# Performance work log

Measured on AMD Instinct MI355X. Metric: run time of the kernel, lower is better.

Reference implementation:

```python
import jax, jax.numpy as jnp
import numpy as np

EPS = 1e-8

def setup_inputs() -> dict:
    key = jax.random.key(0)
    k1, k2, k3 = jax.random.split(key, 3)
    b, c, h, w = 64, 20, 128, 128
    x = jax.random.normal(k1, (b, c, h, w), dtype=jnp.float32)
    y = jax.random.randint(k2, (b, c), 0, 2).astype(jnp.int32)
    threshold_p = jnp.zeros((b, c, h * w), dtype=jnp.float32)
    fg = jax.random.uniform(k3, (b, c), dtype=jnp.float32)
    return {"x": x, "y": y, "threshold_p": threshold_p, "fg": fg, "iter": 0}

def reference(x, y, threshold_p, fg, iter):
    b, c, h, w = x.shape
    hw = h * w
    xs = jax.nn.sigmoid(x.reshape(b, c, hw))  # [b,c,hw]
    yf = y.astype(xs.dtype)
    if iter % 100 < 80:
        # per-row descending sort, pick the fg*(h*w)-th value as threshold
        srt = -jnp.sort(-xs.reshape(b * c, hw), axis=1)  # descending
        idx = (fg.reshape(-1) * hw).astype(jnp.int32)  # [b*c]
        thr = jnp.take_along_axis(srt, idx[:, None], axis=1).reshape(b, c, 1)
        thr = jax.lax.stop_gradient(thr)
    else:
        thr = jax.nn.sigmoid(jnp.mean(threshold_p.reshape(b, c, hw), axis=2))[:, :, None]
        xs = jax.lax.stop_gradient(xs)
    thr = jnp.clip(thr, 0.0001)  # [b,c,1], broadcasts over hw
    y_ = yf[:, :, None]  # [b,c,1] broadcast equivalent of stacking hw copies
    mask_low = jax.lax.stop_gradient((xs <= thr).astype(xs.dtype) * y_)
    mask_high = jax.lax.stop_gradient((xs > thr).astype(xs.dtype) * y_)
    h_low = (-(xs * xs) / (thr * thr) + 2.0 * xs / thr) * mask_low
    alpha = 1.0 / jnp.clip((1.0 - thr) ** 2, EPS)
    h_high = alpha * (1.0 - xs) * (1.0 - 2.0 * thr + xs) * mask_high
    if iter % 100 < 80:
        neg_loss = -(1.0 - y_) * jnp.log(jnp.clip(1.0 - xs, EPS))
        loss = jnp.mean(h_high + h_low + neg_loss)
    else:
        loss = jnp.sum(h_low) / jnp.sum(mask_low) + jnp.sum(h_high) / jnp.sum(mask_high)
    return loss
```

## Files before the change

kernel.cpp:

```cpp
#include <hip/hip_runtime.h>

#define HW     16384
#define NROWS  1280
#define CAPH   1024
#define MB     256

__device__ __forceinline__ unsigned f2u(float f) {
    unsigned u = __float_as_uint(f);
    unsigned m = (unsigned)((int)u >> 31);
    return u ^ (m | 0x80000000u);
}
__device__ __forceinline__ float u2f(unsigned u) {
    u = (u & 0x80000000u) ? (u & 0x7fffffffu) : ~u;
    return __uint_as_float(u);
}

__device__ __forceinline__ float norminv(float p) {
    const float a1=-3.969683028665376e+01f,a2=2.209460984245205e+02f,
                a3=-2.759285104469687e+02f,a4=1.383577518672690e+02f,
                a5=-3.066479806614716e+01f,a6=2.506628277459239e+00f;
    const float b1=-5.447609879822406e+01f,b2=1.615858368580409e+02f,
                b3=-1.556989798598866e+02f,b4=6.680131188771972e+01f,
                b5=-1.328068155288572e+01f;
    const float c1=-7.784894002430293e-03f,c2=-3.223964580411365e-01f,
                c3=-2.400758277161838e+00f,c4=-2.549732539343734e+00f,
                c5=4.374664141464968e+00f,c6=2.938163982698783e+00f;
    const float d1=7.784695709041462e-03f,d2=3.224671290700398e-01f,
                d3=2.445134137142996e+00f,d4=3.754408661907416e+00f;
    const float plow = 0.02425f;
    float q, r;
    if (p < plow) {
        q = sqrtf(-2.f * logf(p));
        return (((((c1*q+c2)*q+c3)*q+c4)*q+c5)*q+c6) /
               ((((d1*q+d2)*q+d3)*q+d4)*q+1.f);
    } else if (p <= 1.f - plow) {
        q = p - 0.5f; r = q * q;
        return (((((a1*r+a2)*r+a3)*r+a4)*r+a5)*r+a6)*q /
               (((((b1*r+b2)*r+b3)*r+b4)*r+b5)*r+1.f);
    } else {
        q = sqrtf(-2.f * logf(1.f - p));
        return -(((((c1*q+c2)*q+c3)*q+c4)*q+c5)*q+c6) /
                ((((d1*q+d2)*q+d3)*q+d4)*q+1.f);
    }
}

__device__ __forceinline__ void bracket_ab(int k, float* fa, float* fb) {
    const float pq  = 1.f - ((float)k + 0.5f) * (1.f / (float)HW);
    const float z   = norminv(pq);
    const float phi = 0.39894228f * exp2f(-0.72134752f * z * z);
    const float sig = sqrtf(pq * (1.f - pq) * (1.f / (float)HW)) / phi;
    const float dl  = 6.f * sig + 0.02f;
    *fa = z + dl; *fb = z - dl;
}

template<int NTH>
__device__ __forceinline__ void block_scan_pick(
    const unsigned* h, int bpl, int stride, unsigned kk,
    volatile unsigned* s_bin, volatile unsigned* s_k, unsigned* wtot)
{
    constexpr int NW = NTH / 64;
    const int tid  = threadIdx.x;
    const int lane = tid & 63;
    const int wid  = tid >> 6;
    const int base = tid * bpl;
    unsigned local = 0;
    for (int j = 0; j < bpl; ++j) {
        int b = base + j;
        local += h[stride * b] + (stride == 2 ? h[stride * b + 1] : 0u);
    }
    unsigned s = local;
    #pragma unroll
    for (int off = 1; off < 64; off <<= 1) {
        unsigned t = __shfl_down(s, off, 64);
        if (lane + off < 64) s += t;
    }
    if (lane == 0) wtot[wid] = s;
    __syncthreads();
    unsigned aw = 0;
    #pragma unroll
    for (int w = 0; w < NW; ++w) if (w > wid) aw += wtot[w];
    const unsigned above = aw + (s - local);
    if (above <= kk && above + local > kk) {
        unsigned run = above;
        for (int j = bpl - 1; j >= 0; --j) {
            int b = base + j;
            unsigned c = h[stride * b] + (stride == 2 ? h[stride * b + 1] : 0u);
            if (run + c > kk) { *s_bin = (unsigned)b; *s_k = kk - run; break; }
            run += c;
        }
    }
    __syncthreads();
}

__global__ __launch_bounds__(256) void stream_pass(
    const float* __restrict__ x, const int* __restrict__ y,
    const float* __restrict__ fg, double* __restrict__ mom,
    unsigned* __restrict__ cnts, unsigned* __restrict__ cand)
{
    __shared__ unsigned sbuf[CAPH];
    __shared__ unsigned s_cnt;
    __shared__ float    swf[4][6];
    __shared__ double   swd[4];

    const int bid  = blockIdx.x;
    const int row  = bid >> 1;
    const int half = bid & 1;
    const int tid  = threadIdx.x;
    const int lane = tid & 63;
    const int wid  = tid >> 6;
    const float4* x4 = (const float4*)(x + (size_t)row * HW + half * (HW / 2));
    const float L2E   = 1.44269504f;
    const float LN2   = 0.69314718f;
    const float NLCAP = 18.420680744f;

    if (y[row] == 0) {
        float a0 = 0.f, a1 = 0.f, a2 = 0.f, a3 = 0.f;
        for (int i = tid; i < HW / 8; i += 256) {
            float4 v = x4[i];
            a0 += fminf(fmaxf(v.x, 0.f) + LN2 * log2f(1.f + exp2f(-L2E * fabsf(v.x))), NLCAP);
            a1 += fminf(fmaxf(v.y, 0.f) + LN2 * log2f(1.f + exp2f(-L2E * fabsf(v.y))), NLCAP);
            a2 += fminf(fmaxf(v.z, 0.f) + LN2 * log2f(1.f + exp2f(-L2E * fabsf(v.z))), NLCAP);
            a3 += fminf(fmaxf(v.w, 0.f) + LN2 * log2f(1.f + exp2f(-L2E * fabsf(v.w))), NLCAP);
        }
        double acc = (double)((a0 + a1) + (a2 + a3));
        #pragma unroll
        for (int off = 32; off > 0; off >>= 1) acc += __shfl_down(acc, off, 64);
        if (lane == 0) swd[wid] = acc;
        __syncthreads();
        if (tid == 0) {
            double t = swd[0] + swd[1] + swd[2] + swd[3];
            mom[(size_t)bid * 6] = t;
        }
        return;
    }

    int k = (int)(fg[row] * (float)HW);
    k = max(0, min(HW - 1, k));
    float fa, fb; bracket_ab(k, &fa, &fb);
    const unsigned ua = f2u(fa), ub = f2u(fb);
    if (tid == 0) s_cnt = 0u;
    __syncthreads();

    float t1a = 0.f, t2a = 0.f, gaa = 0.f, g2aa = 0.f, cafa = 0.f, cbfa = 0.f;
    float t1b = 0.f, t2b = 0.f, gab = 0.f, g2ab = 0.f, cafb = 0.f, cbfb = 0.f;

#define PROC(xv, T1, T2, GA, G2A, CAF, CBF)                                   \
    {                                                                         \
        float _xv = (xv);                                                     \
        unsigned _u = f2u(_xv);                                               \
        float _s = __builtin_amdgcn_rcpf(1.f + exp2f(-L2E * _xv));            \
        float _s2 = _s * _s;                                                  \
        T1 += _s; T2 += _s2;                                                  \
        if (_u > ua) { GA += _s; G2A += _s2; CAF += 1.f; }                    \
        if (_u > ub) {                                                        \
            CBF += 1.f;                                                       \
            if (_u <= ua) {                                                   \
                unsigned _p = atomicAdd(&s_cnt, 1u);                          \
                if (_p < CAPH) sbuf[_p] = _u;                                 \
            }                                                                 \
        }                                                                     \
    }

    for (int i = tid; i < HW / 8; i += 512) {
        float4 v0 = x4[i];
        float4 v1 = x4[i + 256];
        PROC(v0.x, t1a, t2a, gaa, g2aa, cafa, cbfa);
        PROC(v0.y, t1a, t2a, gaa, g2aa, cafa, cbfa);
        PROC(v0.z, t1a, t2a, gaa, g2aa, cafa, cbfa);
        PROC(v0.w, t1a, t2a, gaa, g2aa, cafa, cbfa);
        PROC(v1.x, t1b, t2b, gab, g2ab, cafb, cbfb);
        PROC(v1.y, t1b, t2b, gab, g2ab, cafb, cbfb);
        PROC(v1.z, t1b, t2b, gab, g2ab, cafb, cbfb);
        PROC(v1.w, t1b, t2b, gab, g2ab, cafb, cbfb);
    }
#undef PROC

    float t1 = t1a + t1b, t2 = t2a + t2b;
    float ga = gaa + gab, g2a = g2aa + g2ab;
    float caf = cafa + cafb, cbf = cbfa + cbfb;
    #pragma unroll
    for (int off = 32; off > 0; off >>= 1) {
        t1  += __shfl_down(t1,  off, 64);
        t2  += __shfl_down(t2,  off, 64);
        ga  += __shfl_down(ga,  off, 64);
        g2a += __shfl_down(g2a, off, 64);
        caf += __shfl_down(caf, off, 64);
        cbf += __shfl_down(cbf, off, 64);
    }
    if (lane == 0) {
        swf[wid][0] = t1;  swf[wid][1] = t2;  swf[wid][2] = ga;
        swf[wid][3] = g2a; swf[wid][4] = caf; swf[wid][5] = cbf;
    }
    __syncthreads();
    const unsigned cfin = s_cnt;
    if (tid == 0) {
        double m0 = 0, m1 = 0, m2 = 0, m3 = 0, m4 = 0, m5 = 0;
        #pragma unroll
        for (int w = 0; w < 4; ++w) {
            m0 += swf[w][0]; m1 += swf[w][1]; m2 += swf[w][2];
            m3 += swf[w][3]; m4 += swf[w][4]; m5 += swf[w][5];
        }
        double* o = mom + (size_t)bid * 6;
        o[0] = m0; o[1] = m1; o[2] = m2; o[3] = m3; o[4] = m4; o[5] = m5;
        cnts[bid] = cfin;
    }
    const unsigned c = cfin < CAPH ? cfin : CAPH;
    unsigned* dst = cand + (size_t)bid * CAPH;
    for (unsigned j = tid; j < c; j += 256) dst[j] = sbuf[j];
}

__global__ __launch_bounds__(256) void finalize_row(
    const float* __restrict__ x, const int* __restrict__ y,
    const float* __restrict__ fg, const double* __restrict__ mom,
    const unsigned* __restrict__ cnts, const unsigned* __restrict__ cand,
    double* __restrict__ partial)
{
    __shared__ unsigned hist[4096];
    __shared__ unsigned buf2[MB];
    __shared__ unsigned wtot[4];
    __shared__ unsigned s_cnt2, s_bin, s_k, s_val;
    __shared__ float    swf[4][3];

    const int r    = blockIdx.x;
    const int tid  = threadIdx.x;
    const int lane = tid & 63;
    const int wid  = tid >> 6;

    if (y[r] == 0) {
        if (tid == 0)
            partial[r] = mom[(size_t)(2 * r) * 6] + mom[(size_t)(2 * r + 1) * 6];
        return;
    }

    const double* mA = mom + (size_t)(2 * r) * 6;
    const double* mB = mA + 6;
    const double dS1 = mA[0] + mB[0], dS2 = mA[1] + mB[1];
    const double dGa = mA[2] + mB[2], dG2a = mA[3] + mB[3];
    const double dCa = mA[4] + mB[4], dCb = mA[5] + mB[5];
    const unsigned ca  = (unsigned)(dCa + 0.5);
    const unsigned cbn = (unsigned)(dCb + 0.5);
    int k = (int)(fg[r] * (float)HW);
    k = max(0, min(HW - 1, k));
    const unsigned ku = (unsigned)k;
    const unsigned c0 = cnts[2 * r], c1 = cnts[2 * r + 1];
    const unsigned UCLIP = f2u(-9.2102404f);
    const bool valid = (ca <= ku) && (ku < cbn) && (c0 <= CAPH) && (c1 <= CAPH);
    const unsigned* seg0 = cand + (size_t)(2 * r) * CAPH;
    const unsigned* seg1 = cand + (size_t)(2 * r + 1) * CAPH;
    const unsigned total = c0 + c1;
    const float L2E = 1.44269504f;

    unsigned ustar = 0;
    bool haveU = false;

    if (valid) {
        float fa, fb; bracket_ab(k, &fa, &fb);
        const float scale = 1024.f / (fa - fb);
        for (int i = tid; i < 1024; i += 256) hist[i] = 0u;
        if (tid == 0) s_cnt2 = 0u;
        __syncthreads();
        for (unsigned t = tid; t < total; t += 256) {
            unsigned u = (t < c0) ? seg0[t] : seg1[t - c0];
            int bn = (int)((u2f(u) - fb) * scale);
            bn = max(0, min(1023, bn));
            atomicAdd(&hist[bn], 1u);
        }
        __syncthreads();
        block_scan_pick<256>(hist, 4, 1, ku - ca, &s_bin, &s_k, wtot);
        const unsigned binv = s_bin, kin = s_k;
        for (unsigned t = tid; t < total; t += 256) {
            unsigned u = (t < c0) ? seg0[t] : seg1[t - c0];
            int bn = (int)((u2f(u) - fb) * scale);
            bn = max(0, min(1023, bn));
            if (bn == (int)binv) {
                unsigned p = atomicAdd(&s_cnt2, 1u);
                if (p < MB) buf2[p] = u;
            }
        }
        __syncthreads();
        const unsigned m = s_cnt2;
        if (m <= MB) {
            for (unsigned i = tid; i < m; i += 256) {
                unsigned v = buf2[i];
                unsigned gt = 0, eq = 0;
                for (unsigned j = 0; j < m; ++j) {
                    unsigned w = buf2[j];
                    gt += (w > v); eq += (w == v);
                }
                if (gt <= kin && kin < gt + eq) s_val = v;
            }
        } else {
            const unsigned kp = ku - ca;
            for (unsigned t = tid; t < total; t += 256) {
                unsigned v = (t < c0) ? seg0[t] : seg1[t - c0];
                unsigned gt = 0, eq = 0;
                for (unsigned j = 0; j < total; ++j) {
                    unsigned w = (j < c0) ? seg0[j] : seg1[j - c0];
                    gt += (w > v); eq += (w == v);
                }
                if (gt <= kp && kp < gt + eq) s_val = v;
            }
        }
        __syncthreads();
        ustar = s_val;
        haveU = true;
    }

    float hs = 0.f, hs2 = 0.f, hn = 0.f;
    bool addSide = false;
    if (haveU && ustar >= UCLIP) {
        addSide = true;
        for (unsigned t = tid; t < total; t += 256) {
            unsigned u = (t < c0) ? seg0[t] : seg1[t - c0];
            if (u > ustar) {
                float xv = u2f(u);
                float s = __builtin_amdgcn_rcpf(1.f + exp2f(-L2E * xv));
                hs += s; hs2 += s * s; hn += 1.f;
            }
        }
    } else {
        const float4* x4 = (const float4*)(x + (size_t)r * HW);
        if (!haveU) {
            for (int i = tid; i < 4096; i += 256) hist[i] = 0u;
            __syncthreads();
            for (int i = tid; i < HW / 4; i += 256) {
                float4 v = x4[i];
                atomicAdd(&hist[f2u(v.x) >> 20], 1u);
                atomicAdd(&hist[f2u(v.y) >> 20], 1u);
                atomicAdd(&hist[f2u(v.z) >> 20], 1u);
                atomicAdd(&hist[f2u(v.w) >> 20], 1u);
            }
            __syncthreads();
            block_scan_pick<256>(hist, 16, 1, ku, &s_bin, &s_k, wtot);
            const unsigned bin1 = s_bin, k1 = s_k;
            for (int i = tid; i < 2048; i += 256) hist[i] = 0u;
            __syncthreads();
            for (int i = tid; i < HW / 4; i += 256) {
                float4 v = x4[i];
                unsigned uu[4] = {f2u(v.x), f2u(v.y), f2u(v.z), f2u(v.w)};
                #pragma unroll
                for (int j = 0; j < 4; ++j)
                    if ((uu[j] >> 20) == bin1) atomicAdd(&hist[(uu[j] >> 10) & 1023u], 1u);
            }
            __syncthreads();
            block_scan_pick<256>(hist, 4, 1, k1, &s_bin, &s_k, wtot);
            const unsigned pfx22 = (bin1 << 10) | s_bin;
            const unsigned k2 = s_k;
            for (int i = tid; i < HW / 4; i += 256) {
                float4 v = x4[i];
                unsigned uu[4] = {f2u(v.x), f2u(v.y), f2u(v.z), f2u(v.w)};
                #pragma unroll
                for (int j = 0; j < 4; ++j)
                    if ((uu[j] >> 10) == pfx22) atomicAdd(&hist[1024 + (uu[j] & 1023u)], 1u);
            }
            __syncthreads();
            block_scan_pick<256>(hist + 1024, 4, 1, k2, &s_bin, &s_k, wtot);
            ustar = (pfx22 << 10) | s_bin;
        }
        const unsigned uthr = ustar > UCLIP ? ustar : UCLIP;
        for (int i = tid; i < HW / 4; i += 256) {
            float4 v = x4[i];
            float e[4] = {v.x, v.y, v.z, v.w};
            #pragma unroll
            for (int j = 0; j < 4; ++j) {
                if (f2u(e[j]) > uthr) {
                    float s = __builtin_amdgcn_rcpf(1.f + exp2f(-L2E * e[j]));
                    hs += s; hs2 += s * s; hn += 1.f;
                }
            }
        }
    }

    #pragma unroll
    for (int off = 32; off > 0; off >>= 1) {
        hs  += __shfl_down(hs,  off, 64);
        hs2 += __shfl_down(hs2, off, 64);
        hn  += __shfl_down(hn,  off, 64);
    }
    if (lane == 0) { swf[wid][0] = hs; swf[wid][1] = hs2; swf[wid][2] = hn; }
    __syncthreads();
    if (tid == 0) {
        double HS = 0, HS2 = 0, HN = 0;
        #pragma unroll
        for (int w = 0; w < 4; ++w) {
            HS += swf[w][0]; HS2 += swf[w][1]; HN += swf[w][2];
        }
        double SH, S2H, NH;
        if (addSide) { SH = dGa + HS; S2H = dG2a + HS2; NH = dCa + HN; }
        else         { SH = HS;       S2H = HS2;        NH = HN; }
        const double SL = dS1 - SH, S2L = dS2 - S2H;
        const float xk = u2f(ustar);
        float thrf = 1.0f / (1.0f + expf(-xk));
        thrf = fmaxf(thrf, 1e-4f);
        const double t   = (double)thrf;
        const double omt = 1.0 - t;
        const double al  = 1.0 / fmax(omt * omt, 1e-8);
        partial[r] = 2.0 * SL / t - S2L / (t * t)
                   + al * (NH * (1.0 - 2.0 * t) + 2.0 * t * SH - S2H);
    }
}

__global__ __launch_bounds__(256) void final_reduce(
    const double* __restrict__ partial, float* __restrict__ out)
{
    __shared__ double sred[256];
    double acc = 0.0;
    for (int i = threadIdx.x; i < NROWS; i += 256) acc += partial[i];
    sred[threadIdx.x] = acc;
    __syncthreads();
    for (int off = 128; off > 0; off >>= 1) {
        if (threadIdx.x < off) sred[threadIdx.x] += sred[threadIdx.x + off];
        __syncthreads();
    }
    if (threadIdx.x == 0)
        out[0] = (float)(sred[0] / ((double)NROWS * (double)HW));
}

__global__ __launch_bounds__(512) void mono_row(
    const float* __restrict__ x, const int* __restrict__ y,
    const float* __restrict__ fg, double* __restrict__ partial)
{
    __shared__ unsigned hist[4096 * 2];
    __shared__ unsigned buf[1024];
    __shared__ unsigned wtot[8];
    __shared__ unsigned s_cnt, s_bin, s_k;
    __shared__ float    swf[8][5];
    __shared__ double   swd[8];

    const int row  = blockIdx.x;
    const int tid  = threadIdx.x;
    const int lane = tid & 63;
    const int wid  = tid >> 6;
    const float4* x4 = (const float4*)(x + (size_t)row * HW);
    const float L2E   = 1.44269504f;
    const float LN2   = 0.69314718f;
    const float NLCAP = 18.420680744f;

    const int yrow = y[row];

    if (yrow == 0) {
        float a0 = 0.f, a1 = 0.f, a2 = 0.f, a3 = 0.f;
        for (int i = tid; i < HW / 4; i += 512) {
            float4 v = x4[i];
            a0 += fminf(fmaxf(v.x, 0.f) + LN2 * log2f(1.f + exp2f(-L2E * fabsf(v.x))), NLCAP);
            a1 += fminf(fmaxf(v.y, 0.f) + LN2 * log2f(1.f + exp2f(-L2E * fabsf(v.y))), NLCAP);
            a2 += fminf(fmaxf(v.z, 0.f) + LN2 * log2f(1.f + exp2f(-L2E * fabsf(v.z))), NLCAP);
            a3 += fminf(fmaxf(v.w, 0.f) + LN2 * log2f(1.f + exp2f(-L2E * fabsf(v.w))), NLCAP);
        }
        double acc = (double)((a0 + a1) + (a2 + a3));
        #pragma unroll
        for (int off = 32; off > 0; off >>= 1) acc += __shfl_down(acc, off, 64);
        if (lane == 0) swd[wid] = acc;
        __syncthreads();
        if (tid == 0) {
            double t = 0.0;
            for (int w = 0; w < 8; ++w) t += swd[w];
            partial[row] = t;
        }
        return;
    }

    {
        uint4 z = {0u, 0u, 0u, 0u};
        for (int i = tid; i < 4096 * 2 / 4; i += 512) ((uint4*)hist)[i] = z;
    }
    if (tid == 0) {
        int k = (int)(fg[row] * (float)HW);
        k = max(0, min(HW - 1, k));
        s_k = (unsigned)k; s_cnt = 0u;
    }
    __syncthreads();
    const unsigned k0 = s_k;

    const int rep = tid & 1;
    for (int i = tid; i < HW / 4; i += 1024) {
        float4 v0 = x4[i];
        float4 v1 = x4[i + 512];
        atomicAdd(&hist[2 * (f2u(v0.x) >> 20) + rep], 1u);
        atomicAdd(&hist[2 * (f2u(v0.y) >> 20) + rep], 1u);
        atomicAdd(&hist[2 * (f2u(v0.z) >> 20) + rep], 1u);
        atomicAdd(&hist[2 * (f2u(v0.w) >> 20) + rep], 1u);
        atomicAdd(&hist[2 * (f2u(v1.x) >> 20) + rep], 1u);
        atomicAdd(&hist[2 * (f2u(v1.y) >> 20) + rep], 1u);
        atomicAdd(&hist[2 * (f2u(v1.z) >> 20) + rep], 1u);
        atomicAdd(&hist[2 * (f2u(v1.w) >> 20) + rep], 1u);
    }
    __syncthreads();
    block_scan_pick<512>(hist, 4096 / 512, 2, k0, &s_bin, &s_k, wtot);
    const unsigned bin1 = s_bin;
    const unsigned k1   = s_k;

    for (int i = tid; i < 2048; i += 512) hist[i] = 0u;
    float sL = 0.f, s2L = 0.f, sH = 0.f, s2H = 0.f;
    int nH = 0;
    for (int i = tid; i < HW / 4; i += 512) {
        float4 v = x4[i];
        float e[4] = {v.x, v.y, v.z, v.w};
        #pragma unroll
        for (int j = 0; j < 4; ++j) {
            float xv = e[j];
            unsigned u = f2u(xv);
            unsigned b = u >> 20;
            if (b == bin1) {
                unsigned p = atomicAdd(&s_cnt, 1u);
                if (p < 1024) buf[p] = u;
            } else {
                float s = __builtin_amdgcn_rcpf(1.f + exp2f(-L2E * xv));
                float s2 = s * s;
                if (b > bin1) { sH += s; s2H += s2; ++nH; }
                else          { sL += s; s2L += s2; }
            }
        }
    }
    __syncthreads();
    const unsigned cnt = s_cnt;

    unsigned ustar;
    if (cnt <= 1024) {
        for (int c = tid; c < (int)cnt; c += 512)
            atomicAdd(&hist[(buf[c] >> 10) & 1023u], 1u);
        __syncthreads();
        block_scan_pick<512>(hist, 2, 1, k1, &s_bin, &s_k, wtot);
        const unsigned pfx22 = (bin1 << 10) | s_bin;
        const unsigned k2    = s_k;
        for (int c = tid; c < (int)cnt; c += 512)
            if ((buf[c] >> 10) == pfx22) atomicAdd(&hist[1024 + (buf[c] & 1023u)], 1u);
        __syncthreads();
        block_scan_pick<512>(hist + 1024, 2, 1, k2, &s_bin, &s_k, wtot);
        ustar = (pfx22 << 10) | s_bin;
    } else {
        for (int i = tid; i < HW / 4; i += 512) {
            float4 v = x4[i];
            unsigned uu[4] = {f2u(v.x), f2u(v.y), f2u(v.z), f2u(v.w)};
            #pragma unroll
            for (int j = 0; j < 4; ++j)
                if ((uu[j] >> 20) == bin1) atomicAdd(&hist[(uu[j] >> 10) & 1023u], 1u);
        }
        __syncthreads();
        block_scan_pick<512>(hist, 2, 1, k1, &s_bin, &s_k, wtot);
        const unsigned pfx22 = (bin1 << 10) | s_bin;
        const unsigned k2    = s_k;
        for (int i = tid; i < HW / 4; i += 512) {
            float4 v = x4[i];
            unsigned uu[4] = {f2u(v.x), f2u(v.y), f2u(v.z), f2u(v.w)};
            #pragma unroll
            for (int j = 0; j < 4; ++j)
                if ((uu[j] >> 10) == pfx22) atomicAdd(&hist[1024 + (uu[j] & 1023u)], 1u);
        }
        __syncthreads();
        block_scan_pick<512>(hist + 1024, 2, 1, k2, &s_bin, &s_k, wtot);
        ustar = (pfx22 << 10) | s_bin;
    }

    const float xk = u2f(ustar);
    float thr = 1.0f / (1.0f + expf(-xk));
    thr = fmaxf(thr, 1e-4f);

    if (cnt <= 1024) {
        for (int c = tid; c < (int)cnt; c += 512) {
            float xv = u2f(buf[c]);
            float s  = __builtin_amdgcn_rcpf(1.f + exp2f(-L2E * xv));
            float s2 = s * s;
            if (s > thr) { sH += s; s2H += s2; ++nH; }
            else         { sL += s; s2L += s2; }
        }
    } else {
        for (int i = tid; i < HW / 4; i += 512) {
            float4 v = x4[i];
            float e[4] = {v.x, v.y, v.z, v.w};
            #pragma unroll
            for (int j = 0; j < 4; ++j) {
                unsigned u = f2u(e[j]);
                if ((u >> 20) == bin1) {
                    float s  = __builtin_amdgcn_rcpf(1.f + exp2f(-L2E * e[j]));
                    float s2 = s * s;
                    if (s > thr) { sH += s; s2H += s2; ++nH; }
                    else         { sL += s; s2L += s2; }
                }
            }
        }
    }

    float nHf = (float)nH;
    #pragma unroll
    for (int off = 32; off > 0; off >>= 1) {
        sL  += __shfl_down(sL,  off, 64);
        s2L += __shfl_down(s2L, off, 64);
        sH  += __shfl_down(sH,  off, 64);
        s2H += __shfl_down(s2H, off, 64);
        nHf += __shfl_down(nHf, off, 64);
    }
    if (lane == 0) {
        swf[wid][0] = sL; swf[wid][1] = s2L; swf[wid][2] = sH;
        swf[wid][3] = s2H; swf[wid][4] = nHf;
    }
    __syncthreads();
    if (tid == 0) {
        double SL = 0, S2L = 0, SH = 0, S2H = 0, NH = 0;
        for (int w = 0; w < 8; ++w) {
            SL += swf[w][0]; S2L += swf[w][1]; SH += swf[w][2];
            S2H += swf[w][3]; NH += (double)swf[w][4];
        }
        const double t   = (double)thr;
        const double omt = 1.0 - t;
        const double al  = 1.0 / fmax(omt * omt, 1e-8);
        partial[row] = 2.0 * SL / t - S2L / (t * t)
                     + al * (NH * (1.0 - 2.0 * t) + 2.0 * t * SH - S2H);
    }
}

extern "C" void kernel_launch(void* const* d_in, const int* in_sizes, int n_in,
                              void* d_out, int out_size, void* d_ws, size_t ws_size,
                              hipStream_t stream) {
    const float* x  = (const float*)d_in[0];
    const int*   y  = (const int*)d_in[1];
    const float* fg = (const float*)d_in[3];

    const size_t offPartial = 0;
    const size_t offMom     = offPartial + (size_t)NROWS * 8;
    const size_t offCnts    = offMom + (size_t)2 * NROWS * 6 * 8;
    const size_t offCand    = offCnts + (size_t)2 * NROWS * 4;
    const size_t need       = offCand + (size_t)2 * NROWS * CAPH * 4;

    double* partial = (double*)((char*)d_ws + offPartial);

    if (ws_size >= need) {
        double*   mom  = (double*)((char*)d_ws + offMom);
        unsigned* cnts = (unsigned*)((char*)d_ws + offCnts);
        unsigned* cand = (unsigned*)((char*)d_ws + offCand);
        stream_pass <<<2 * NROWS, 256, 0, stream>>>(x, y, fg, mom, cnts, cand);
        finalize_row<<<NROWS,     256, 0, stream>>>(x, y, fg, mom, cnts, cand, partial);
        final_reduce<<<1,         256, 0, stream>>>(partial, (float*)d_out);
    } else {
        mono_row    <<<NROWS, 512, 0, stream>>>(x, y, fg, partial);
        final_reduce<<<1,     256, 0, stream>>>(partial, (float*)d_out);
    }
}
```

Before: 39.57 us.

## Split rows into quarter-segment tasks and fuse final reduction via last-block counter

The streaming pass now splits each row into four segments handled as tasks, with 512 threads per block and a fixed number of tasks per block. Candidate values are written straight to global memory with a smaller per-segment cap instead of being staged in LDS. The finalize kernel merges the four segment moments, builds the threshold histogram from candidates, and performs the global reduction itself through a done counter, which removes the separate final_reduce launch. This trades an extra memset and atomic global writes for finer work distribution and one fewer kernel launch; the smaller cap may send more rows to the full-scan fallback.

```diff
diff --git a/kernel.cpp b/kernel.cpp
--- a/kernel.cpp
+++ b/kernel.cpp
@@ -2,7 +2,14 @@
 
 #define HW     16384
 #define NROWS  1280
-#define CAPH   1024
+#define SEGSR  4
+#define SEGLEN (HW / SEGSR)
+#define NTASKS (NROWS * SEGSR)
+#define NB1    1024
+#define NT1    512
+#define TPB    (NTASKS / NB1)
+#define CAPQ   512
+#define NT2    256
 #define MB     256
 
 __device__ __forceinline__ unsigned f2u(float f) {
@@ -55,7 +62,7 @@
 
 template<int NTH>
 __device__ __forceinline__ void block_scan_pick(
-    const unsigned* h, int bpl, int stride, unsigned kk,
+    const unsigned* h, int bpl, unsigned kk,
     volatile unsigned* s_bin, volatile unsigned* s_k, unsigned* wtot)
 {
     constexpr int NW = NTH / 64;
@@ -64,10 +71,7 @@
     const int wid  = tid >> 6;
     const int base = tid * bpl;
     unsigned local = 0;
-    for (int j = 0; j < bpl; ++j) {
-        int b = base + j;
-        local += h[stride * b] + (stride == 2 ? h[stride * b + 1] : 0u);
-    }
+    for (int j = 0; j < bpl; ++j) local += h[base + j];
     unsigned s = local;
     #pragma unroll
     for (int off = 1; off < 64; off <<= 1) {
@@ -83,337 +87,346 @@
     if (above <= kk && above + local > kk) {
         unsigned run = above;
         for (int j = bpl - 1; j >= 0; --j) {
-            int b = base + j;
-            unsigned c = h[stride * b] + (stride == 2 ? h[stride * b + 1] : 0u);
-            if (run + c > kk) { *s_bin = (unsigned)b; *s_k = kk - run; break; }
+            unsigned c = h[base + j];
+            if (run + c > kk) { *s_bin = (unsigned)(base + j); *s_k = kk - run; break; }
             run += c;
         }
     }
     __syncthreads();
 }
 
-__global__ __launch_bounds__(256) void stream_pass(
+__global__ __launch_bounds__(NT1, 8) void stream_tasks(
     const float* __restrict__ x, const int* __restrict__ y,
     const float* __restrict__ fg, double* __restrict__ mom,
     unsigned* __restrict__ cnts, unsigned* __restrict__ cand)
 {
-    __shared__ unsigned sbuf[CAPH];
     __shared__ unsigned s_cnt;
-    __shared__ float    swf[4][6];
-    __shared__ double   swd[4];
-
-    const int bid  = blockIdx.x;
-    const int row  = bid >> 1;
-    const int half = bid & 1;
+    __shared__ float    swf[8][6];
+    __shared__ double   swd[8];
+
     const int tid  = threadIdx.x;
     const int lane = tid & 63;
     const int wid  = tid >> 6;
-    const float4* x4 = (const float4*)(x + (size_t)row * HW + half * (HW / 2));
     const float L2E   = 1.44269504f;
     const float LN2   = 0.69314718f;
     const float NLCAP = 18.420680744f;
 
-    if (y[row] == 0) {
-        float a0 = 0.f, a1 = 0.f, a2 = 0.f, a3 = 0.f;
-        for (int i = tid; i < HW / 8; i += 256) {
-            float4 v = x4[i];
-            a0 += fminf(fmaxf(v.x, 0.f) + LN2 * log2f(1.f + exp2f(-L2E * fabsf(v.x))), NLCAP);
-            a1 += fminf(fmaxf(v.y, 0.f) + LN2 * log2f(1.f + exp2f(-L2E * fabsf(v.y))), NLCAP);
-            a2 += fminf(fmaxf(v.z, 0.f) + LN2 * log2f(1.f + exp2f(-L2E * fabsf(v.z))), NLCAP);
-            a3 += fminf(fmaxf(v.w, 0.f) + LN2 * log2f(1.f + exp2f(-L2E * fabsf(v.w))), NLCAP);
-        }
-        double acc = (double)((a0 + a1) + (a2 + a3));
-        #pragma unroll
-        for (int off = 32; off > 0; off >>= 1) acc += __shfl_down(acc, off, 64);
-        if (lane == 0) swd[wid] = acc;
-        __syncthreads();
-        if (tid == 0) {
-            double t = swd[0] + swd[1] + swd[2] + swd[3];
-            mom[(size_t)bid * 6] = t;
-        }
-        return;
-    }
-
-    int k = (int)(fg[row] * (float)HW);
-    k = max(0, min(HW - 1, k));
-    float fa, fb; bracket_ab(k, &fa, &fb);
-    const unsigned ua = f2u(fa), ub = f2u(fb);
-    if (tid == 0) s_cnt = 0u;
-    __syncthreads();
-
-    float t1a = 0.f, t2a = 0.f, gaa = 0.f, g2aa = 0.f, cafa = 0.f, cbfa = 0.f;
-    float t1b = 0.f, t2b = 0.f, gab = 0.f, g2ab = 0.f, cafb = 0.f, cbfb = 0.f;
-
-#define PROC(xv, T1, T2, GA, G2A, CAF, CBF)                                   \
-    {                                                                         \
-        float _xv = (xv);                                                     \
-        unsigned _u = f2u(_xv);                                               \
-        float _s = __builtin_amdgcn_rcpf(1.f + exp2f(-L2E * _xv));            \
-        float _s2 = _s * _s;                                                  \
-        T1 += _s; T2 += _s2;                                                  \
-        if (_u > ua) { GA += _s; G2A += _s2; CAF += 1.f; }                    \
-        if (_u > ub) {                                                        \
-            CBF += 1.f;                                                       \
-            if (_u <= ua) {                                                   \
-                unsigned _p = atomicAdd(&s_cnt, 1u);                          \
-                if (_p < CAPH) sbuf[_p] = _u;                                 \
-            }                                                                 \
-        }                                                                     \
-    }
-
-    for (int i = tid; i < HW / 8; i += 512) {
-        float4 v0 = x4[i];
-        float4 v1 = x4[i + 256];
-        PROC(v0.x, t1a, t2a, gaa, g2aa, cafa, cbfa);
-        PROC(v0.y, t1a, t2a, gaa, g2aa, cafa, cbfa);
-        PROC(v0.z, t1a, t2a, gaa, g2aa, cafa, cbfa);
-        PROC(v0.w, t1a, t2a, gaa, g2aa, cafa, cbfa);
-        PROC(v1.x, t1b, t2b, gab, g2ab, cafb, cbfb);
-        PROC(v1.y, t1b, t2b, gab, g2ab, cafb, cbfb);
-        PROC(v1.z, t1b, t2b, gab, g2ab, cafb, cbfb);
-        PROC(v1.w, t1b, t2b, gab, g2ab, cafb, cbfb);
-    }
-#undef PROC
-
-    float t1 = t1a + t1b, t2 = t2a + t2b;
-    float ga = gaa + gab, g2a = g2aa + g2ab;
-    float caf = cafa + cafb, cbf = cbfa + cbfb;
-    #pragma unroll
-    for (int off = 32; off > 0; off >>= 1) {
-        t1  += __shfl_down(t1,  off, 64);
-        t2  += __shfl_down(t2,  off, 64);
-        ga  += __shfl_down(ga,  off, 64);
-        g2a += __shfl_down(g2a, off, 64);
-        caf += __shfl_down(caf, off, 64);
-        cbf += __shfl_down(cbf, off, 64);
-    }
-    if (lane == 0) {
-        swf[wid][0] = t1;  swf[wid][1] = t2;  swf[wid][2] = ga;
-        swf[wid][3] = g2a; swf[wid][4] = caf; swf[wid][5] = cbf;
-    }
-    __syncthreads();
-    const unsigned cfin = s_cnt;
-    if (tid == 0) {
-        double m0 = 0, m1 = 0, m2 = 0, m3 = 0, m4 = 0, m5 = 0;
-        #pragma unroll
-        for (int w = 0; w < 4; ++w) {
-            m0 += swf[w][0]; m1 += swf[w][1]; m2 += swf[w][2];
-            m3 += swf[w][3]; m4 += swf[w][4]; m5 += swf[w][5];
-        }
-        double* o = mom + (size_t)bid * 6;
-        o[0] = m0; o[1] = m1; o[2] = m2; o[3] = m3; o[4] = m4; o[5] = m5;
-        cnts[bid] = cfin;
-    }
-    const unsigned c = cfin < CAPH ? cfin : CAPH;
-    unsigned* dst = cand + (size_t)bid * CAPH;
-    for (unsigned j = tid; j < c; j += 256) dst[j] = sbuf[j];
-}
-
-__global__ __launch_bounds__(256) void finalize_row(
+    const int t0 = blockIdx.x * TPB;
+    for (int t = t0; t < t0 + TPB; ++t) {
+        const int row = t >> 2;
+        const int seg = t & 3;
+        const float4* x4 = (const float4*)(x + (size_t)row * HW + seg * SEGLEN);
+        const int yrow = y[row];
+
+        __syncthreads();
+        if (yrow == 0) {
+            float4 v0 = x4[tid];
+            float4 v1 = x4[tid + NT1];
+            float a = 0.f;
+            a += fminf(fmaxf(v0.x, 0.f) + LN2 * log2f(1.f + exp2f(-L2E * fabsf(v0.x))), NLCAP);
+            a += fminf(fmaxf(v0.y, 0.f) + LN2 * log2f(1.f + exp2f(-L2E * fabsf(v0.y))), NLCAP);
+            a += fminf(fmaxf(v0.z, 0.f) + LN2 * log2f(1.f + exp2f(-L2E * fabsf(v0.z))), NLCAP);
+            a += fminf(fmaxf(v0.w, 0.f) + LN2 * log2f(1.f + exp2f(-L2E * fabsf(v0.w))), NLCAP);
+            a += fminf(fmaxf(v1.x, 0.f) + LN2 * log2f(1.f + exp2f(-L2E * fabsf(v1.x))), NLCAP);
+            a += fminf(fmaxf(v1.y, 0.f) + LN2 * log2f(1.f + exp2f(-L2E * fabsf(v1.y))), NLCAP);
+            a += fminf(fmaxf(v1.z, 0.f) + LN2 * log2f(1.f + exp2f(-L2E * fabsf(v1.z))), NLCAP);
+            a += fminf(fmaxf(v1.w, 0.f) + LN2 * log2f(1.f + exp2f(-L2E * fabsf(v1.w))), NLCAP);
+            #pragma unroll
+            for (int off = 32; off > 0; off >>= 1) a += __shfl_down(a, off, 64);
+            if (lane == 0) swd[wid] = (double)a;
+            __syncthreads();
+            if (tid == 0) {
+                double s = 0.0;
+                #pragma unroll
+                for (int w = 0; w < 8; ++w) s += swd[w];
+                mom[(size_t)t * 6] = s;
+            }
+        } else {
+            int k = (int)(fg[row] * (float)HW);
+            k = max(0, min(HW - 1, k));
+            float fa, fb; bracket_ab(k, &fa, &fb);
+            const unsigned ua = f2u(fa), ub = f2u(fb);
+            if (tid == 0) s_cnt = 0u;
+            __syncthreads();
+
+            unsigned* dst = cand + (size_t)t * CAPQ;
+            float t1 = 0.f, t2 = 0.f, ga = 0.f, g2a = 0.f, caf = 0.f, cbf = 0.f;
+            float4 v0 = x4[tid];
+            float4 v1 = x4[tid + NT1];
+            float e[8] = {v0.x, v0.y, v0.z, v0.w, v1.x, v1.y, v1.z, v1.w};
+            #pragma unroll
+            for (int j = 0; j < 8; ++j) {
+                float xv = e[j];
+                unsigned u = f2u(xv);
+                float s = __builtin_amdgcn_rcpf(1.f + exp2f(-L2E * xv));
+                float s2 = s * s;
+                t1 += s; t2 += s2;
+                if (u > ua) { ga += s; g2a += s2; caf += 1.f; }
+                if (u > ub) {
+                    cbf += 1.f;
+                    if (u <= ua) {
+                        unsigned p = atomicAdd(&s_cnt, 1u);
+                        if (p < CAPQ) dst[p] = u;
+                    }
+                }
+            }
+            #pragma unroll
+            for (int off = 32; off > 0; off >>= 1) {
+                t1  += __shfl_down(t1,  off, 64);
+                t2  += __shfl_down(t2,  off, 64);
+                ga  += __shfl_down(ga,  off, 64);
+                g2a += __shfl_down(g2a, off, 64);
+                caf += __shfl_down(caf, off, 64);
+                cbf += __shfl_down(cbf, off, 64);
+            }
+            if (lane == 0) {
+                swf[wid][0] = t1;  swf[wid][1] = t2;  swf[wid][2] = ga;
+                swf[wid][3] = g2a; swf[wid][4] = caf; swf[wid][5] = cbf;
+            }
+            __syncthreads();
+            if (tid == 0) {
+                double m0 = 0, m1 = 0, m2 = 0, m3 = 0, m4 = 0, m5 = 0;
+                #pragma unroll
+                for (int w = 0; w < 8; ++w) {
+                    m0 += swf[w][0]; m1 += swf[w][1]; m2 += swf[w][2];
+                    m3 += swf[w][3]; m4 += swf[w][4]; m5 += swf[w][5];
+                }
+                double* o = mom + (size_t)t * 6;
+                o[0] = m0; o[1] = m1; o[2] = m2; o[3] = m3; o[4] = m4; o[5] = m5;
+                cnts[t] = s_cnt;
+            }
+        }
+    }
+}
+
+__global__ __launch_bounds__(NT2) void finalize_row(
     const float* __restrict__ x, const int* __restrict__ y,
     const float* __restrict__ fg, const double* __restrict__ mom,
     const unsigned* __restrict__ cnts, const unsigned* __restrict__ cand,
-    double* __restrict__ partial)
+    double* __restrict__ partial, unsigned* __restrict__ done,
+    float* __restrict__ out)
 {
     __shared__ unsigned hist[4096];
     __shared__ unsigned buf2[MB];
-    __shared__ unsigned wtot[4];
-    __shared__ unsigned s_cnt2, s_bin, s_k, s_val;
-    __shared__ float    swf[4][3];
+    __shared__ unsigned wtot[NT2 / 64];
+    __shared__ unsigned s_cnt2, s_bin, s_k, s_val, s_last;
+    __shared__ float    swf[NT2 / 64][3];
+    __shared__ double   sred[NT2];
 
     const int r    = blockIdx.x;
     const int tid  = threadIdx.x;
     const int lane = tid & 63;
     const int wid  = tid >> 6;
+    const float L2E = 1.44269504f;
 
     if (y[r] == 0) {
+        if (tid == 0) {
+            const double* m = mom + (size_t)(4 * r) * 6;
+            partial[r] = m[0] + m[6] + m[12] + m[18];
+        }
+    } else {
+        const double* m0 = mom + (size_t)(4 * r) * 6;
+        double dS1 = 0, dS2 = 0, dGa = 0, dG2a = 0, dCa = 0, dCb = 0;
+        #pragma unroll
+        for (int s = 0; s < 4; ++s) {
+            const double* m = m0 + s * 6;
+            dS1 += m[0]; dS2 += m[1]; dGa += m[2];
+            dG2a += m[3]; dCa += m[4]; dCb += m[5];
+        }
+        const unsigned ca  = (unsigned)(dCa + 0.5);
+        const unsigned cbn = (unsigned)(dCb + 0.5);
+        int k = (int)(fg[r] * (float)HW);
+        k = max(0, min(HW - 1, k));
+        const unsigned ku = (unsigned)k;
+        unsigned c[4];
+        #pragma unroll
+        for (int s = 0; s < 4; ++s) c[s] = cnts[4 * r + s];
+        const unsigned UCLIP = f2u(-9.2102404f);
+        const bool capok = (c[0] <= CAPQ) && (c[1] <= CAPQ) &&
+                           (c[2] <= CAPQ) && (c[3] <= CAPQ);
+        const bool valid = (ca <= ku) && (ku < cbn) && capok;
+        const unsigned* seg[4];
+        #pragma unroll
+        for (int s = 0; s < 4; ++s) seg[s] = cand + (size_t)(4 * r + s) * CAPQ;
+
+        unsigned ustar = 0;
+        bool haveU = false;
+
+        if (valid) {
+            float fa, fb; bracket_ab(k, &fa, &fb);
+            const float scale = 1024.f / (fa - fb);
+            const unsigned kp = ku - ca;
+            for (int i = tid; i < 1024; i += NT2) hist[i] = 0u;
+            if (tid == 0) s_cnt2 = 0u;
+            __syncthreads();
+            #pragma unroll
+            for (int s = 0; s < 4; ++s)
+                for (unsigned j = tid; j < c[s]; j += NT2) {
+                    int bn = (int)((u2f(seg[s][j]) - fb) * scale);
+                    bn = max(0, min(1023, bn));
+                    atomicAdd(&hist[bn], 1u);
+                }
+            __syncthreads();
+            block_scan_pick<NT2>(hist, 1024 / NT2, kp, &s_bin, &s_k, wtot);
+            const unsigned binv = s_bin, kin = s_k;
+            #pragma unroll
+            for (int s = 0; s < 4; ++s)
+                for (unsigned j = tid; j < c[s]; j += NT2) {
+                    unsigned u = seg[s][j];
+                    int bn = (int)((u2f(u) - fb) * scale);
+                    bn = max(0, min(1023, bn));
+                    if (bn == (int)binv) {
+                        unsigned p = atomicAdd(&s_cnt2, 1u);
+                        if (p < MB) buf2[p] = u;
+                    }
+                }
+            __syncthreads();
+            const unsigned m = s_cnt2;
+            if (m <= MB) {
+                for (unsigned i = tid; i < m; i += NT2) {
+                    unsigned v = buf2[i];
+                    unsigned gt = 0, eq = 0;
+                    for (unsigned j = 0; j < m; ++j) {
+                        unsigned w = buf2[j];
+                        gt += (w > v); eq += (w == v);
+                    }
+                    if (gt <= kin && kin < gt + eq) s_val = v;
+                }
+            } else {
+                const unsigned total = c[0] + c[1] + c[2] + c[3];
+                for (unsigned ti = tid; ti < total; ti += NT2) {
+                    unsigned idx = ti, ss = 0;
+                    while (idx >= c[ss]) { idx -= c[ss]; ++ss; }
+                    unsigned v = seg[ss][idx];
+                    unsigned gt = 0, eq = 0;
+                    for (int s2 = 0; s2 < 4; ++s2)
+                        for (unsigned j = 0; j < c[s2]; ++j) {
+                            unsigned w = seg[s2][j];
+                            gt += (w > v); eq += (w == v);
+                        }
+                    if (gt <= kp && kp < gt + eq) s_val = v;
+                }
+            }
+            __syncthreads();
+            ustar = s_val;
+            haveU = true;
+        }
+
+        float hs = 0.f, hs2 = 0.f, hn = 0.f;
+        bool addSide = false;
+        if (haveU && ustar >= UCLIP) {
+            addSide = true;
+            #pragma unroll
+            for (int s = 0; s < 4; ++s)
+                for (unsigned j = tid; j < c[s]; j += NT2) {
+                    unsigned u = seg[s][j];
+                    if (u > ustar) {
+                        float sg = __builtin_amdgcn_rcpf(1.f + exp2f(-L2E * u2f(u)));
+                        hs += sg; hs2 += sg * sg; hn += 1.f;
+                    }
+                }
+        } else {
+            const float4* x4 = (const float4*)(x + (size_t)r * HW);
+            if (!haveU) {
+                for (int i = tid; i < 4096; i += NT2) hist[i] = 0u;
+                __syncthreads();
+                for (int i = tid; i < HW / 4; i += NT2) {
+                    float4 v = x4[i];
+                    atomicAdd(&hist[f2u(v.x) >> 20], 1u);
+                    atomicAdd(&hist[f2u(v.y) >> 20], 1u);
+                    atomicAdd(&hist[f2u(v.z) >> 20], 1u);
+                    atomicAdd(&hist[f2u(v.w) >> 20], 1u);
+                }
+                __syncthreads();
+                block_scan_pick<NT2>(hist, 16, ku, &s_bin, &s_k, wtot);
+                const unsigned bin1 = s_bin, k1 = s_k;
+                for (int i = tid; i < 2048; i += NT2) hist[i] = 0u;
+                __syncthreads();
+                for (int i = tid; i < HW / 4; i += NT2) {
+                    float4 v = x4[i];
+                    unsigned uu[4] = {f2u(v.x), f2u(v.y), f2u(v.z), f2u(v.w)};
+                    #pragma unroll
+                    for (int j = 0; j < 4; ++j)
+                        if ((uu[j] >> 20) == bin1) atomicAdd(&hist[(uu[j] >> 10) & 1023u], 1u);
+                }
+                __syncthreads();
+                block_scan_pick<NT2>(hist, 4, k1, &s_bin, &s_k, wtot);
+                const unsigned pfx22 = (bin1 << 10) | s_bin;
+                const unsigned k2 = s_k;
+                for (int i = tid; i < HW / 4; i += NT2) {
+                    float4 v = x4[i];
+                    unsigned uu[4] = {f2u(v.x), f2u(v.y), f2u(v.z), f2u(v.w)};
+                    #pragma unroll
+                    for (int j = 0; j < 4; ++j)
+                        if ((uu[j] >> 10) == pfx22) atomicAdd(&hist[1024 + (uu[j] & 1023u)], 1u);
+                }
+                __syncthreads();
+                block_scan_pick<NT2>(hist + 1024, 4, k2, &s_bin, &s_k, wtot);
+                ustar = (pfx22 << 10) | s_bin;
+            }
+            const unsigned uthr = ustar > UCLIP ? ustar : UCLIP;
+            for (int i = tid; i < HW / 4; i += NT2) {
+                float4 v = x4[i];
+                float e[4] = {v.x, v.y, v.z, v.w};
+                #pragma unroll
+                for (int j = 0; j < 4; ++j) {
+                    if (f2u(e[j]) > uthr) {
+                        float sg = __builtin_amdgcn_rcpf(1.f + exp2f(-L2E * e[j]));
+                        hs += sg; hs2 += sg * sg; hn += 1.f;
+                    }
+                }
+            }
+        }
+
+        #pragma unroll
+        for (int off = 32; off > 0; off >>= 1) {
+            hs  += __shfl_down(hs,  off, 64);
+            hs2 += __shfl_down(hs2, off, 64);
+            hn  += __shfl_down(hn,  off, 64);
+        }
+        if (lane == 0) { swf[wid][0] = hs; swf[wid][1] = hs2; swf[wid][2] = hn; }
+        __syncthreads();
+        if (tid == 0) {
+            double HS = 0, HS2 = 0, HN = 0;
+            #pragma unroll
+            for (int w = 0; w < NT2 / 64; ++w) {
+                HS += swf[w][0]; HS2 += swf[w][1]; HN += swf[w][2];
+            }
+            double SH, S2H, NH;
+            if (addSide) { SH = dGa + HS; S2H = dG2a + HS2; NH = dCa + HN; }
+            else         { SH = HS;       S2H = HS2;        NH = HN; }
+            const double SL = dS1 - SH, S2L = dS2 - S2H;
+            const float xk = u2f(ustar);
+            float thrf = 1.0f / (1.0f + expf(-xk));
+            thrf = fmaxf(thrf, 1e-4f);
+            const double t   = (double)thrf;
+            const double omt = 1.0 - t;
+            const double al  = 1.0 / fmax(omt * omt, 1e-8);
+            partial[r] = 2.0 * SL / t - S2L / (t * t)
+                       + al * (NH * (1.0 - 2.0 * t) + 2.0 * t * SH - S2H);
+        }
+    }
+
+    __syncthreads();
+    if (tid == 0) {
+        __threadfence();
+        unsigned old = atomicAdd(done, 1u);
+        s_last = (old == NROWS - 1) ? 1u : 0u;
+    }
+    __syncthreads();
+    if (s_last) {
+        __threadfence();
+        double a = 0.0;
+        for (int i = tid; i < NROWS; i += NT2) a += partial[i];
+        sred[tid] = a;
+        __syncthreads();
+        for (int off = NT2 / 2; off > 0; off >>= 1) {
+            if (tid < off) sred[tid] += sred[tid + off];
+            __syncthreads();
+        }
         if (tid == 0)
-            partial[r] = mom[(size_t)(2 * r) * 6] + mom[(size_t)(2 * r + 1) * 6];
-        return;
-    }
-
-    const double* mA = mom + (size_t)(2 * r) * 6;
-    const double* mB = mA + 6;
-    const double dS1 = mA[0] + mB[0], dS2 = mA[1] + mB[1];
-    const double dGa = mA[2] + mB[2], dG2a = mA[3] + mB[3];
-    const double dCa = mA[4] + mB[4], dCb = mA[5] + mB[5];
-    const unsigned ca  = (unsigned)(dCa + 0.5);
-    const unsigned cbn = (unsigned)(dCb + 0.5);
-    int k = (int)(fg[r] * (float)HW);
-    k = max(0, min(HW - 1, k));
-    const unsigned ku = (unsigned)k;
-    const unsigned c0 = cnts[2 * r], c1 = cnts[2 * r + 1];
-    const unsigned UCLIP = f2u(-9.2102404f);
-    const bool valid = (ca <= ku) && (ku < cbn) && (c0 <= CAPH) && (c1 <= CAPH);
-    const unsigned* seg0 = cand + (size_t)(2 * r) * CAPH;
-    const unsigned* seg1 = cand + (size_t)(2 * r + 1) * CAPH;
-    const unsigned total = c0 + c1;
-    const float L2E = 1.44269504f;
-
-    unsigned ustar = 0;
-    bool haveU = false;
-
-    if (valid) {
-        float fa, fb; bracket_ab(k, &fa, &fb);
-        const float scale = 1024.f / (fa - fb);
-        for (int i = tid; i < 1024; i += 256) hist[i] = 0u;
-        if (tid == 0) s_cnt2 = 0u;
-        __syncthreads();
-        for (unsigned t = tid; t < total; t += 256) {
-            unsigned u = (t < c0) ? seg0[t] : seg1[t - c0];
-            int bn = (int)((u2f(u) - fb) * scale);
-            bn = max(0, min(1023, bn));
-            atomicAdd(&hist[bn], 1u);
-        }
-        __syncthreads();
-        block_scan_pick<256>(hist, 4, 1, ku - ca, &s_bin, &s_k, wtot);
-        const unsigned binv = s_bin, kin = s_k;
-        for (unsigned t = tid; t < total; t += 256) {
-            unsigned u = (t < c0) ? seg0[t] : seg1[t - c0];
-            int bn = (int)((u2f(u) - fb) * scale);
-            bn = max(0, min(1023, bn));
-            if (bn == (int)binv) {
-                unsigned p = atomicAdd(&s_cnt2, 1u);
-                if (p < MB) buf2[p] = u;
-            }
-        }
-        __syncthreads();
-        const unsigned m = s_cnt2;
-        if (m <= MB) {
-            for (unsigned i = tid; i < m; i += 256) {
-                unsigned v = buf2[i];
-                unsigned gt = 0, eq = 0;
-                for (unsigned j = 0; j < m; ++j) {
-                    unsigned w = buf2[j];
-                    gt += (w > v); eq += (w == v);
-                }
-                if (gt <= kin && kin < gt + eq) s_val = v;
-            }
-        } else {
-            const unsigned kp = ku - ca;
-            for (unsigned t = tid; t < total; t += 256) {
-                unsigned v = (t < c0) ? seg0[t] : seg1[t - c0];
-                unsigned gt = 0, eq = 0;
-                for (unsigned j = 0; j < total; ++j) {
-                    unsigned w = (j < c0) ? seg0[j] : seg1[j - c0];
-                    gt += (w > v); eq += (w == v);
-                }
-                if (gt <= kp && kp < gt + eq) s_val = v;
-            }
-        }
-        __syncthreads();
-        ustar = s_val;
-        haveU = true;
-    }
-
-    float hs = 0.f, hs2 = 0.f, hn = 0.f;
-    bool addSide = false;
-    if (haveU && ustar >= UCLIP) {
-        addSide = true;
-        for (unsigned t = tid; t < total; t += 256) {
-            unsigned u = (t < c0) ? seg0[t] : seg1[t - c0];
-            if (u > ustar) {
-                float xv = u2f(u);
-                float s = __builtin_amdgcn_rcpf(1.f + exp2f(-L2E * xv));
-                hs += s; hs2 += s * s; hn += 1.f;
-            }
-        }
-    } else {
-        const float4* x4 = (const float4*)(x + (size_t)r * HW);
-        if (!haveU) {
-            for (int i = tid; i < 4096; i += 256) hist[i] = 0u;
-            __syncthreads();
-            for (int i = tid; i < HW / 4; i += 256) {
-                float4 v = x4[i];
-                atomicAdd(&hist[f2u(v.x) >> 20], 1u);
-                atomicAdd(&hist[f2u(v.y) >> 20], 1u);
-                atomicAdd(&hist[f2u(v.z) >> 20], 1u);
-                atomicAdd(&hist[f2u(v.w) >> 20], 1u);
-            }
-            __syncthreads();
-            block_scan_pick<256>(hist, 16, 1, ku, &s_bin, &s_k, wtot);
-            const unsigned bin1 = s_bin, k1 = s_k;
-            for (int i = tid; i < 2048; i += 256) hist[i] = 0u;
-            __syncthreads();
-            for (int i = tid; i < HW / 4; i += 256) {
-                float4 v = x4[i];
-                unsigned uu[4] = {f2u(v.x), f2u(v.y), f2u(v.z), f2u(v.w)};
-                #pragma unroll
-                for (int j = 0; j < 4; ++j)
-                    if ((uu[j] >> 20) == bin1) atomicAdd(&hist[(uu[j] >> 10) & 1023u], 1u);
-            }
-            __syncthreads();
-            block_scan_pick<256>(hist, 4, 1, k1, &s_bin, &s_k, wtot);
-            const unsigned pfx22 = (bin1 << 10) | s_bin;
-            const unsigned k2 = s_k;
-            for (int i = tid; i < HW / 4; i += 256) {
-                float4 v = x4[i];
-                unsigned uu[4] = {f2u(v.x), f2u(v.y), f2u(v.z), f2u(v.w)};
-                #pragma unroll
-                for (int j = 0; j < 4; ++j)
-                    if ((uu[j] >> 10) == pfx22) atomicAdd(&hist[1024 + (uu[j] & 1023u)], 1u);
-            }
-            __syncthreads();
-            block_scan_pick<256>(hist + 1024, 4, 1, k2, &s_bin, &s_k, wtot);
-            ustar = (pfx22 << 10) | s_bin;
-        }
-        const unsigned uthr = ustar > UCLIP ? ustar : UCLIP;
-        for (int i = tid; i < HW / 4; i += 256) {
-            float4 v = x4[i];
-            float e[4] = {v.x, v.y, v.z, v.w};
-            #pragma unroll
-            for (int j = 0; j < 4; ++j) {
-                if (f2u(e[j]) > uthr) {
-                    float s = __builtin_amdgcn_rcpf(1.f + exp2f(-L2E * e[j]));
-                    hs += s; hs2 += s * s; hn += 1.f;
-                }
-            }
-        }
-    }
-
-    #pragma unroll
-    for (int off = 32; off > 0; off >>= 1) {
-        hs  += __shfl_down(hs,  off, 64);
-        hs2 += __shfl_down(hs2, off, 64);
-        hn  += __shfl_down(hn,  off, 64);
-    }
-    if (lane == 0) { swf[wid][0] = hs; swf[wid][1] = hs2; swf[wid][2] = hn; }
-    __syncthreads();
-    if (tid == 0) {
-        double HS = 0, HS2 = 0, HN = 0;
-        #pragma unroll
-        for (int w = 0; w < 4; ++w) {
-            HS += swf[w][0]; HS2 += swf[w][1]; HN += swf[w][2];
-        }
-        double SH, S2H, NH;
-        if (addSide) { SH = dGa + HS; S2H = dG2a + HS2; NH = dCa + HN; }
-        else         { SH = HS;       S2H = HS2;        NH = HN; }
-        const double SL = dS1 - SH, S2L = dS2 - S2H;
-        const float xk = u2f(ustar);
-        float thrf = 1.0f / (1.0f + expf(-xk));
-        thrf = fmaxf(thrf, 1e-4f);
-        const double t   = (double)thrf;
-        const double omt = 1.0 - t;
-        const double al  = 1.0 / fmax(omt * omt, 1e-8);
-        partial[r] = 2.0 * SL / t - S2L / (t * t)
-                   + al * (NH * (1.0 - 2.0 * t) + 2.0 * t * SH - S2H);
-    }
-}
-
-__global__ __launch_bounds__(256) void final_reduce(
-    const double* __restrict__ partial, float* __restrict__ out)
-{
-    __shared__ double sred[256];
-    double acc = 0.0;
-    for (int i = threadIdx.x; i < NROWS; i += 256) acc += partial[i];
-    sred[threadIdx.x] = acc;
-    __syncthreads();
-    for (int off = 128; off > 0; off >>= 1) {
-        if (threadIdx.x < off) sred[threadIdx.x] += sred[threadIdx.x + off];
-        __syncthreads();
-    }
-    if (threadIdx.x == 0)
-        out[0] = (float)(sred[0] / ((double)NROWS * (double)HW));
+            out[0] = (float)(sred[0] / ((double)NROWS * (double)HW));
+    }
 }
 
 __global__ __launch_bounds__(512) void mono_row(
@@ -437,7 +450,6 @@
     const float NLCAP = 18.420680744f;
 
     const int yrow = y[row];
-
     if (yrow == 0) {
         float a0 = 0.f, a1 = 0.f, a2 = 0.f, a3 = 0.f;
         for (int i = tid; i < HW / 4; i += 512) {
@@ -459,7 +471,6 @@
         }
         return;
     }
-
     {
         uint4 z = {0u, 0u, 0u, 0u};
         for (int i = tid; i < 4096 * 2 / 4; i += 512) ((uint4*)hist)[i] = z;
@@ -471,7 +482,6 @@
     }
     __syncthreads();
     const unsigned k0 = s_k;
-
     const int rep = tid & 1;
     for (int i = tid; i < HW / 4; i += 1024) {
         float4 v0 = x4[i];
@@ -486,10 +496,36 @@
         atomicAdd(&hist[2 * (f2u(v1.w) >> 20) + rep], 1u);
     }
     __syncthreads();
-    block_scan_pick<512>(hist, 4096 / 512, 2, k0, &s_bin, &s_k, wtot);
+    {
+        const int bpl = 4096 / 512;
+        const int base = tid * bpl;
+        unsigned local = 0;
+        for (int j = 0; j < bpl; ++j)
+            local += hist[2 * (base + j)] + hist[2 * (base + j) + 1];
+        unsigned s = local;
+        #pragma unroll
+        for (int off = 1; off < 64; off <<= 1) {
+            unsigned t = __shfl_down(s, off, 64);
+            if (lane + off < 64) s += t;
+        }
+        if (lane == 0) wtot[wid] = s;
+        __syncthreads();
+        unsigned aw = 0;
+        #pragma unroll
+        for (int w = 0; w < 8; ++w) if (w > wid) aw += wtot[w];
+        const unsigned above = aw + (s - local);
+        if (above <= k0 && above + local > k0) {
+            unsigned run = above;
+            for (int j = bpl - 1; j >= 0; --j) {
+                unsigned cbin = hist[2 * (base + j)] + hist[2 * (base + j) + 1];
+                if (run + cbin > k0) { s_bin = (unsigned)(base + j); s_k = k0 - run; break; }
+                run += cbin;
+            }
+        }
+        __syncthreads();
+    }
     const unsigned bin1 = s_bin;
     const unsigned k1   = s_k;
-
     for (int i = tid; i < 2048; i += 512) hist[i] = 0u;
     float sL = 0.f, s2L = 0.f, sH = 0.f, s2H = 0.f;
     int nH = 0;
@@ -498,14 +534,13 @@
         float e[4] = {v.x, v.y, v.z, v.w};
         #pragma unroll
         for (int j = 0; j < 4; ++j) {
-            float xv = e[j];
-            unsigned u = f2u(xv);
+            unsigned u = f2u(e[j]);
             unsigned b = u >> 20;
             if (b == bin1) {
                 unsigned p = atomicAdd(&s_cnt, 1u);
                 if (p < 1024) buf[p] = u;
             } else {
-                float s = __builtin_amdgcn_rcpf(1.f + exp2f(-L2E * xv));
+                float s = __builtin_amdgcn_rcpf(1.f + exp2f(-L2E * e[j]));
                 float s2 = s * s;
                 if (b > bin1) { sH += s; s2H += s2; ++nH; }
                 else          { sL += s; s2L += s2; }
@@ -514,19 +549,18 @@
     }
     __syncthreads();
     const unsigned cnt = s_cnt;
-
     unsigned ustar;
     if (cnt <= 1024) {
-        for (int c = tid; c < (int)cnt; c += 512)
-            atomicAdd(&hist[(buf[c] >> 10) & 1023u], 1u);
-        __syncthreads();
-        block_scan_pick<512>(hist, 2, 1, k1, &s_bin, &s_k, wtot);
+        for (int c2 = tid; c2 < (int)cnt; c2 += 512)
+            atomicAdd(&hist[(buf[c2] >> 10) & 1023u], 1u);
+        __syncthreads();
+        block_scan_pick<512>(hist, 2, k1, &s_bin, &s_k, wtot);
         const unsigned pfx22 = (bin1 << 10) | s_bin;
-        const unsigned k2    = s_k;
-        for (int c = tid; c < (int)cnt; c += 512)
-            if ((buf[c] >> 10) == pfx22) atomicAdd(&hist[1024 + (buf[c] & 1023u)], 1u);
-        __syncthreads();
-        block_scan_pick<512>(hist + 1024, 2, 1, k2, &s_bin, &s_k, wtot);
+        const unsigned k2 = s_k;
+        for (int c2 = tid; c2 < (int)cnt; c2 += 512)
+            if ((buf[c2] >> 10) == pfx22) atomicAdd(&hist[1024 + (buf[c2] & 1023u)], 1u);
+        __syncthreads();
+        block_scan_pick<512>(hist + 1024, 2, k2, &s_bin, &s_k, wtot);
         ustar = (pfx22 << 10) | s_bin;
     } else {
         for (int i = tid; i < HW / 4; i += 512) {
@@ -537,9 +571,9 @@
                 if ((uu[j] >> 20) == bin1) atomicAdd(&hist[(uu[j] >> 10) & 1023u], 1u);
         }
         __syncthreads();
-        block_scan_pick<512>(hist, 2, 1, k1, &s_bin, &s_k, wtot);
+        block_scan_pick<512>(hist, 2, k1, &s_bin, &s_k, wtot);
         const unsigned pfx22 = (bin1 << 10) | s_bin;
-        const unsigned k2    = s_k;
+        const unsigned k2 = s_k;
         for (int i = tid; i < HW / 4; i += 512) {
             float4 v = x4[i];
             unsigned uu[4] = {f2u(v.x), f2u(v.y), f2u(v.z), f2u(v.w)};
@@ -548,17 +582,15 @@
                 if ((uu[j] >> 10) == pfx22) atomicAdd(&hist[1024 + (uu[j] & 1023u)], 1u);
         }
         __syncthreads();
-        block_scan_pick<512>(hist + 1024, 2, 1, k2, &s_bin, &s_k, wtot);
+        block_scan_pick<512>(hist + 1024, 2, k2, &s_bin, &s_k, wtot);
         ustar = (pfx22 << 10) | s_bin;
     }
-
     const float xk = u2f(ustar);
     float thr = 1.0f / (1.0f + expf(-xk));
     thr = fmaxf(thr, 1e-4f);
-
     if (cnt <= 1024) {
-        for (int c = tid; c < (int)cnt; c += 512) {
-            float xv = u2f(buf[c]);
+        for (int c2 = tid; c2 < (int)cnt; c2 += 512) {
+            float xv = u2f(buf[c2]);
             float s  = __builtin_amdgcn_rcpf(1.f + exp2f(-L2E * xv));
             float s2 = s * s;
             if (s > thr) { sH += s; s2H += s2; ++nH; }
@@ -580,7 +612,6 @@
             }
         }
     }
-
     float nHf = (float)nH;
     #pragma unroll
     for (int off = 32; off > 0; off >>= 1) {
@@ -609,6 +640,22 @@
     }
 }
 
+__global__ __launch_bounds__(256) void final_reduce(
+    const double* __restrict__ partial, float* __restrict__ out)
+{
+    __shared__ double sred[256];
+    double acc = 0.0;
+    for (int i = threadIdx.x; i < NROWS; i += 256) acc += partial[i];
+    sred[threadIdx.x] = acc;
+    __syncthreads();
+    for (int off = 128; off > 0; off >>= 1) {
+        if (threadIdx.x < off) sred[threadIdx.x] += sred[threadIdx.x + off];
+        __syncthreads();
+    }
+    if (threadIdx.x == 0)
+        out[0] = (float)(sred[0] / ((double)NROWS * (double)HW));
+}
+
 extern "C" void kernel_launch(void* const* d_in, const int* in_sizes, int n_in,
                               void* d_out, int out_size, void* d_ws, size_t ws_size,
                               hipStream_t stream) {
@@ -618,19 +665,22 @@
 
     const size_t offPartial = 0;
     const size_t offMom     = offPartial + (size_t)NROWS * 8;
-    const size_t offCnts    = offMom + (size_t)2 * NROWS * 6 * 8;
-    const size_t offCand    = offCnts + (size_t)2 * NROWS * 4;
-    const size_t need       = offCand + (size_t)2 * NROWS * CAPH * 4;
+    const size_t offCnts    = offMom + (size_t)NTASKS * 6 * 8;
+    const size_t offDone    = offCnts + (size_t)NTASKS * 4;
+    const size_t offCand    = offDone + 256;
+    const size_t need       = offCand + (size_t)NTASKS * CAPQ * 4;
 
     double* partial = (double*)((char*)d_ws + offPartial);
 
     if (ws_size >= need) {
         double*   mom  = (double*)((char*)d_ws + offMom);
         unsigned* cnts = (unsigned*)((char*)d_ws + offCnts);
+        unsigned* done = (unsigned*)((char*)d_ws + offDone);
         unsigned* cand = (unsigned*)((char*)d_ws + offCand);
-        stream_pass <<<2 * NROWS, 256, 0, stream>>>(x, y, fg, mom, cnts, cand);
-        finalize_row<<<NROWS,     256, 0, stream>>>(x, y, fg, mom, cnts, cand, partial);
-        final_reduce<<<1,         256, 0, stream>>>(partial, (float*)d_out);
+        hipMemsetAsync(done, 0, sizeof(unsigned), stream);
+        stream_tasks<<<NB1,   NT1, 0, stream>>>(x, y, fg, mom, cnts, cand);
+        finalize_row<<<NROWS, NT2, 0, stream>>>(x, y, fg, mom, cnts, cand,
+                                                partial, done, (float*)d_out);
     } else {
         mono_row    <<<NROWS, 512, 0, stream>>>(x, y, fg, partial);
         final_reduce<<<1,     256, 0, stream>>>(partial, (float*)d_out);
```

Result: slower. 74.33 us (+87.9%).
